# Performance work log

Hardware: AMD Instinct MI355X
Metric: run time of the kernel (lower is better)

The kernel has to match this reference:

```python
import jax, jax.numpy as jnp
import numpy as np

N_TREES, DEPTH, INPUT_DIM, N_CLASSES = 15, 3, 128, 10
N_LEAVES = 2 ** DEPTH
N_INTERNAL = N_LEAVES - 1


def _path_masks(depth):
    """Right/left ancestor indicator matrices [n_leaves, n_internal]."""
    n_leaves = 2 ** depth
    n_int = n_leaves - 1
    R = np.zeros((n_leaves, n_int), np.float32)
    L = np.zeros((n_leaves, n_int), np.float32)
    for leaf in range(n_leaves):
        node = leaf + n_int
        for _ in range(depth):
            parent = (node - 1) // 2
            if node % 2 == 0:
                R[leaf, parent] = 1.0
            else:
                L[leaf, parent] = 1.0
            node = parent
    return R, L

_R, _L = _path_masks(DEPTH)


def setup_inputs() -> dict:
    key = jax.random.key(0)
    k1, k2 = jax.random.split(key)
    batch = 262144
    per_tree = N_INTERNAL * INPUT_DIM + N_INTERNAL + N_LEAVES * N_CLASSES
    total = N_TREES * per_tree + N_TREES
    x = jax.random.normal(k1, (batch, INPUT_DIM), dtype=jnp.float32)
    params = jax.random.normal(k2, (total,), dtype=jnp.float32)
    return {"x": x, "params": params}


def reference(x, params):
    per_tree = N_INTERNAL * INPUT_DIM + N_INTERNAL + N_LEAVES * N_CLASSES
    blocks = params[: N_TREES * per_tree].reshape(N_TREES, per_tree)
    w_end = N_INTERNAL * INPUT_DIM
    split_w = blocks[:, :w_end].reshape(N_TREES, N_INTERNAL, INPUT_DIM)
    split_b = blocks[:, w_end : w_end + N_INTERNAL]  # [T, n_internal]
    leaf_logits = blocks[:, w_end + N_INTERNAL :].reshape(N_TREES, N_LEAVES, N_CLASSES)
    tree_w_logits = params[N_TREES * per_tree :]  # [T]

    # split logits z: [B, T, n_internal]
    z = jnp.einsum("bd,tnd->btn", x, split_w) + split_b[None, :, :]
    log_p = jax.nn.log_sigmoid(z)        # log sigma(z)
    log_1mp = jax.nn.log_sigmoid(-z)     # log (1 - sigma(z))

    R = jnp.asarray(_R)
    L = jnp.asarray(_L)
    # path product in log domain: [B, T, n_leaves]
    leaf_probs = jnp.exp(
        jnp.einsum("btn,ln->btl", log_p, R) + jnp.einsum("btn,ln->btl", log_1mp, L)
    )

    leaf_class_probs = jax.nn.softmax(leaf_logits, axis=-1)  # [T, n_leaves, C]
    tree_pred = jnp.einsum("btl,tlc->btc", leaf_probs, leaf_class_probs)
    tree_weights = jax.nn.softmax(tree_w_logits, axis=0)     # [T]
    final_pred = jnp.einsum("btc,t->bc", tree_pred, tree_weights)
    return final_pred
```

## Files before the change

### kernel.cpp

```cpp
#include <hip/hip_runtime.h>
#include <hip/hip_fp16.h>


typedef float    f32x4 __attribute__((ext_vector_type(4)));
typedef _Float16 half8 __attribute__((ext_vector_type(8)));

#define TREES      15
#define IDIM       128
#define NCLS       10
#define NINT       7
#define NLVS       8
#define PER_TREE   (NINT*IDIM + NINT + NLVS*NCLS)
#define NODES      (TREES*NINT)
#define NPAD       112
#define KPAD       128
#define RSTR       272
#define NBLK       512

__global__ __launch_bounds__(256) void prep_kernel(const float* __restrict__ p,
                                                   _Float16* __restrict__ wq,
                                                   float* __restrict__ bq,
                                                   _Float16* __restrict__ wbT) {
    const int gid  = blockIdx.x * 256 + threadIdx.x;
    const int nthr = gridDim.x * 256;

    for (int i = gid; i < NPAD * IDIM; i += nthr) {
        int g = i >> 7, k = i & 127;
        float v = 0.f;
        if (g < NODES) {
            int t = g / NINT, n = g % NINT;
            v = p[t * PER_TREE + n * IDIM + k];
        }
        wq[i] = (_Float16)v;
    }
    for (int i = gid; i < NPAD; i += nthr) {
        float v = 0.f;
        if (i < NODES) {
            int t = i / NINT, n = i % NINT;
            v = p[t * PER_TREE + NINT * IDIM + n];
        }
        bq[i] = v;
    }
    const float* tl = p + TREES * PER_TREE;
    for (int i = gid; i < 16 * KPAD; i += nthr) {
        int c = i >> 7, k = i & 127;
        float v = 0.f;
        if (c < NCLS && k < TREES * NLVS) {
            int t = k >> 3, l = k & 7;
            const float* ll = p + t * PER_TREE + NINT * IDIM + NINT + l * NCLS;
            float mx = ll[0];
            #pragma unroll
            for (int j = 1; j < NCLS; ++j) mx = fmaxf(mx, ll[j]);
            float se = 0.f;
            #pragma unroll
            for (int j = 0; j < NCLS; ++j) se += __expf(ll[j] - mx);
            float lsm = __expf(ll[c] - mx) / se;

            float m2 = tl[0];
            #pragma unroll
            for (int j = 1; j < TREES; ++j) m2 = fmaxf(m2, tl[j]);
            float s2 = 0.f;
            #pragma unroll
            for (int j = 0; j < TREES; ++j) s2 += __expf(tl[j] - m2);
            float tw = __expf(tl[t] - m2) / s2;
            v = lsm * tw;
        }
        wbT[i] = (_Float16)v;
    }
}

__device__ __forceinline__ void dma_quarter(const float* __restrict__ x,
                                            long grow0, char* qdst, int lane) {
    const int slot = lane & 31;
    #pragma unroll
    for (int it = 0; it < 8; ++it) {
        int r   = 2 * it + (lane >> 5);
        int c16 = (slot - r) & 31;
        const float* gp = x + (grow0 + r) * IDIM + c16 * 4;
        __builtin_amdgcn_global_load_lds(
            (const __attribute__((address_space(1))) void*)gp,
            (__attribute__((address_space(3))) void*)(qdst + it * 1024),
            16, 0, 0);
    }
}

__global__ __launch_bounds__(256, 2) void tree_main(const float* __restrict__ x,
                                                    const _Float16* __restrict__ wq,
                                                    const float* __restrict__ bq,
                                                    const _Float16* __restrict__ wbT,
                                                    float* __restrict__ out,
                                                    int tpb) {
    __shared__ __align__(16) char lds[2][32768];

    const int tid  = threadIdx.x;
    const int lane = tid & 63;
    const int w    = tid >> 6;
    const int lm   = lane & 15;
    const int lq   = lane >> 4;
    const int rg   = lane >> 2;
    const int g    = lane & 3;

    const long tile0 = (long)blockIdx.x * tpb;

    dma_quarter(x, tile0 * 64 + 16 * w, &lds[0][w * 8192], lane);

    half8 bf[7][4];
    float bb[7];
    #pragma unroll
    for (int nt = 0; nt < 7; ++nt) {
        bb[nt] = bq[16 * nt + lm];
        #pragma unroll
        for (int s = 0; s < 4; ++s)
            bf[nt][s] = *reinterpret_cast<const half8*>(wq + (16 * nt + lm) * IDIM + 32 * s + 8 * lq);
    }
    half8 wbf[4];
    #pragma unroll
    for (int s = 0; s < 4; ++s)
        wbf[s] = *reinterpret_cast<const half8*>(wbT + lm * KPAD + 32 * s + 8 * lq);

    for (int i = 0; i < tpb; ++i) {
        char* qcur = &lds[i & 1][w * 8192];
        const long grow = (tile0 + i) * 64;

        asm volatile("" ::: "memory");
        __builtin_amdgcn_s_waitcnt(0x0F70);
        asm volatile("" ::: "memory");

        half8 af[4];
        #pragma unroll
        for (int s = 0; s < 4; ++s) {
            int cc = 8 * s + 2 * lq;
            f32x4 f0 = *(const f32x4*)(qcur + lm * 512 + (((cc     + lm) & 31) << 4));
            f32x4 f1 = *(const f32x4*)(qcur + lm * 512 + (((cc + 1 + lm) & 31) << 4));
            half8 a;
            #pragma unroll
            for (int j = 0; j < 4; ++j) {
                a[j]     = (_Float16)f0[j];
                a[j + 4] = (_Float16)f1[j];
            }
            af[s] = a;
        }

        if (i + 1 < tpb)
            dma_quarter(x, (tile0 + i + 1) * 64 + 16 * w, &lds[(i + 1) & 1][w * 8192], lane);

        #pragma unroll
        for (int nt = 0; nt < 7; ++nt) {
            f32x4 acc = {0.f, 0.f, 0.f, 0.f};
            #pragma unroll
            for (int s = 0; s < 4; ++s)
                acc = __builtin_amdgcn_mfma_f32_16x16x32_f16(af[s], bf[nt][s], acc, 0, 0, 0);
            int node = 16 * nt + lm;
            int col  = node + ((node * 9363) >> 16);
            #pragma unroll
            for (int r = 0; r < 4; ++r) {
                float z  = acc[r] + bb[nt];
                float sg = __builtin_amdgcn_rcpf(1.0f + __expf(-z));
                *(_Float16*)(qcur + (4 * lq + r) * RSTR + col * 2) = (_Float16)sg;
            }
        }

        {
            const char* rowp = qcur + rg * RSTR;
            float sgv[4][7];
            #pragma unroll
            for (int tt = 0; tt < 4; ++tt) {
                int t = 4 * g + tt;
                #pragma unroll
                for (int n = 0; n < 7; ++n)
                    sgv[tt][n] = (float)*(const _Float16*)(rowp + (8 * t + n) * 2);
            }
            half8 lv[4];
            #pragma unroll
            for (int tt = 0; tt < 4; ++tt) {
                float s0 = sgv[tt][0], s1 = sgv[tt][1], s2 = sgv[tt][2];
                float s3 = sgv[tt][3], s4 = sgv[tt][4], s5 = sgv[tt][5], s6 = sgv[tt][6];
                float u1 = 1.f - s0, u2 = s0;
                float q1 = u1 * s1, q0 = u1 - q1;
                float q3 = u2 * s2, q2 = u2 - q3;
                float L1 = q0 * s3, L0 = q0 - L1;
                float L3 = q1 * s4, L2 = q1 - L3;
                float L5 = q2 * s5, L4 = q2 - L5;
                float L7 = q3 * s6, L6 = q3 - L7;
                float m = (4 * g + tt < TREES) ? 1.f : 0.f;
                half8 lv8;
                lv8[0] = (_Float16)(L0 * m); lv8[1] = (_Float16)(L1 * m);
                lv8[2] = (_Float16)(L2 * m); lv8[3] = (_Float16)(L3 * m);
                lv8[4] = (_Float16)(L4 * m); lv8[5] = (_Float16)(L5 * m);
                lv8[6] = (_Float16)(L6 * m); lv8[7] = (_Float16)(L7 * m);
                lv[tt] = lv8;
            }
            #pragma unroll
            for (int tt = 0; tt < 4; ++tt)
                *(half8*)(qcur + rg * RSTR + 64 * g + 16 * tt) = lv[tt];
        }

        {
            half8 af2[4];
            #pragma unroll
            for (int s = 0; s < 4; ++s)
                af2[s] = *(const half8*)(qcur + lm * RSTR + 64 * s + 16 * lq);
            f32x4 a2 = {0.f, 0.f, 0.f, 0.f};
            #pragma unroll
            for (int s = 0; s < 4; ++s)
                a2 = __builtin_amdgcn_mfma_f32_16x16x32_f16(af2[s], wbf[s], a2, 0, 0, 0);
            if (lm < NCLS) {
                #pragma unroll
                for (int r = 0; r < 4; ++r)
                    out[(grow + 16 * w + 4 * lq + r) * NCLS + lm] = a2[r];
            }
        }
    }
}

extern "C" void kernel_launch(void* const* d_in, const int* in_sizes, int n_in,
                              void* d_out, int out_size, void* d_ws, size_t ws_size,
                              hipStream_t stream) {
    const float* x      = (const float*)d_in[0];
    const float* params = (const float*)d_in[1];
    float* out = (float*)d_out;

    _Float16* wq  = (_Float16*)d_ws;
    float*    bq  = (float*)((char*)d_ws + NPAD * IDIM * 2);
    _Float16* wbT = (_Float16*)((char*)bq + NPAD * 4);

    const int batch = in_sizes[0] / IDIM;
    const int tiles = batch / 64;
    const int tpb   = tiles / NBLK;

    prep_kernel<<<8, 256, 0, stream>>>(params, wq, bq, wbT);
    tree_main<<<NBLK, 256, 0, stream>>>(x, wq, bq, wbT, out, tpb);
}
```

Baseline: 204.3 us.

## Use padded LDS row layout and unroll double-buffer loop by two

Replaces the rotated-column swizzle of the staged x tile in LDS with a plain layout. Pairs of 512-byte rows are padded to a 1040-byte stride, so the DMA and gather address math becomes simpler. The main loop is manually unrolled by two with fixed A/B buffers, and the explicit s_waitcnt before the gather is removed, so ordering of the LDS DMA now depends on the compiler. The unroll assumes an even tiles-per-block count. Bank-conflict behaviour of the new padding may differ from the old swizzle.

```diff
diff --git a/kernel.cpp b/kernel.cpp
--- a/kernel.cpp
+++ b/kernel.cpp
@@ -15,6 +15,8 @@
 #define NPAD       112
 #define KPAD       128
 #define RSTR       272
+#define QSTR       1040
+#define QSZ        (8 * QSTR)
 #define NBLK       512
 
 __global__ __launch_bounds__(256) void prep_kernel(const float* __restrict__ p,
@@ -71,15 +73,12 @@
 
 __device__ __forceinline__ void dma_quarter(const float* __restrict__ x,
                                             long grow0, char* qdst, int lane) {
-    const int slot = lane & 31;
     #pragma unroll
     for (int it = 0; it < 8; ++it) {
-        int r   = 2 * it + (lane >> 5);
-        int c16 = (slot - r) & 31;
-        const float* gp = x + (grow0 + r) * IDIM + c16 * 4;
+        const float* gp = x + (grow0 + 2 * it + (lane >> 5)) * IDIM + (lane & 31) * 4;
         __builtin_amdgcn_global_load_lds(
             (const __attribute__((address_space(1))) void*)gp,
-            (__attribute__((address_space(3))) void*)(qdst + it * 1024),
+            (__attribute__((address_space(3))) void*)(qdst + it * QSTR),
             16, 0, 0);
     }
 }
@@ -90,7 +89,8 @@
                                                     const _Float16* __restrict__ wbT,
                                                     float* __restrict__ out,
                                                     int tpb) {
-    __shared__ __align__(16) char lds[2][32768];
+    __shared__ __align__(16) char ldsA[4 * QSZ];
+    __shared__ __align__(16) char ldsB[4 * QSZ];
 
     const int tid  = threadIdx.x;
     const int lane = tid & 63;
@@ -100,9 +100,12 @@
     const int rg   = lane >> 2;
     const int g    = lane & 3;
 
+    char* qA = &ldsA[w * QSZ];
+    char* qB = &ldsB[w * QSZ];
+
     const long tile0 = (long)blockIdx.x * tpb;
 
-    dma_quarter(x, tile0 * 64 + 16 * w, &lds[0][w * 8192], lane);
+    dma_quarter(x, tile0 * 64 + 16 * w, qA, lane);
 
     half8 bf[7][4];
     float bb[7];
@@ -118,20 +121,12 @@
     for (int s = 0; s < 4; ++s)
         wbf[s] = *reinterpret_cast<const half8*>(wbT + lm * KPAD + 32 * s + 8 * lq);
 
-    for (int i = 0; i < tpb; ++i) {
-        char* qcur = &lds[i & 1][w * 8192];
-        const long grow = (tile0 + i) * 64;
-
-        asm volatile("" ::: "memory");
-        __builtin_amdgcn_s_waitcnt(0x0F70);
-        asm volatile("" ::: "memory");
-
-        half8 af[4];
+    auto gather = [&](const char* q, half8 af[4]) {
         #pragma unroll
         for (int s = 0; s < 4; ++s) {
-            int cc = 8 * s + 2 * lq;
-            f32x4 f0 = *(const f32x4*)(qcur + lm * 512 + (((cc     + lm) & 31) << 4));
-            f32x4 f1 = *(const f32x4*)(qcur + lm * 512 + (((cc + 1 + lm) & 31) << 4));
+            const char* p0 = q + (lm >> 1) * QSTR + (lm & 1) * 512 + 128 * s + 32 * lq;
+            f32x4 f0 = *(const f32x4*)(p0);
+            f32x4 f1 = *(const f32x4*)(p0 + 16);
             half8 a;
             #pragma unroll
             for (int j = 0; j < 4; ++j) {
@@ -140,10 +135,9 @@
             }
             af[s] = a;
         }
-
-        if (i + 1 < tpb)
-            dma_quarter(x, (tile0 + i + 1) * 64 + 16 * w, &lds[(i + 1) & 1][w * 8192], lane);
-
+    };
+
+    auto compute = [&](char* q, const half8 af[4], long grow) {
         #pragma unroll
         for (int nt = 0; nt < 7; ++nt) {
             f32x4 acc = {0.f, 0.f, 0.f, 0.f};
@@ -156,19 +150,18 @@
             for (int r = 0; r < 4; ++r) {
                 float z  = acc[r] + bb[nt];
                 float sg = __builtin_amdgcn_rcpf(1.0f + __expf(-z));
-                *(_Float16*)(qcur + (4 * lq + r) * RSTR + col * 2) = (_Float16)sg;
+                *(_Float16*)(q + (4 * lq + r) * RSTR + col * 2) = (_Float16)sg;
             }
         }
 
         {
-            const char* rowp = qcur + rg * RSTR;
+            const char* rowp = q + rg * RSTR;
             float sgv[4][7];
             #pragma unroll
             for (int tt = 0; tt < 4; ++tt) {
-                int t = 4 * g + tt;
                 #pragma unroll
                 for (int n = 0; n < 7; ++n)
-                    sgv[tt][n] = (float)*(const _Float16*)(rowp + (8 * t + n) * 2);
+                    sgv[tt][n] = (float)*(const _Float16*)(rowp + (8 * (4 * g + tt) + n) * 2);
             }
             half8 lv[4];
             #pragma unroll
@@ -192,14 +185,14 @@
             }
             #pragma unroll
             for (int tt = 0; tt < 4; ++tt)
-                *(half8*)(qcur + rg * RSTR + 64 * g + 16 * tt) = lv[tt];
+                *(half8*)(q + rg * RSTR + 64 * g + 16 * tt) = lv[tt];
         }
 
         {
             half8 af2[4];
             #pragma unroll
             for (int s = 0; s < 4; ++s)
-                af2[s] = *(const half8*)(qcur + lm * RSTR + 64 * s + 16 * lq);
+                af2[s] = *(const half8*)(q + lm * RSTR + 64 * s + 16 * lq);
             f32x4 a2 = {0.f, 0.f, 0.f, 0.f};
             #pragma unroll
             for (int s = 0; s < 4; ++s)
@@ -210,6 +203,18 @@
                     out[(grow + 16 * w + 4 * lq + r) * NCLS + lm] = a2[r];
             }
         }
+    };
+
+    for (int i = 0; i < tpb; i += 2) {
+        half8 af[4];
+        gather(qA, af);
+        dma_quarter(x, (tile0 + i + 1) * 64 + 16 * w, qB, lane);
+        compute(qA, af, (tile0 + i) * 64);
+
+        gather(qB, af);
+        if (i + 2 < tpb)
+            dma_quarter(x, (tile0 + i + 2) * 64 + 16 * w, qA, lane);
+        compute(qB, af, (tile0 + i + 1) * 64);
     }
 }
 
```

Result: no change. 204.8 us (+0.2%).
